# Optimization experiments

Measured on AMD Instinct MI355X. Metric: run time of the kernel, lower is better.

## Reference

```python
import jax, jax.numpy as jnp
import numpy as np
import math

NUM_HEADS = 8

def setup_inputs() -> dict:
    key = jax.random.key(0)
    k1, k2, k3 = jax.random.split(key, 3)
    B, N, C = 16, 4096, 512
    x = jax.random.normal(k1, (B, N, C), dtype=jnp.float32)
    qkv_w = jax.random.normal(k2, (3 * C, C), dtype=jnp.float32) * 0.02
    proj_w = jax.random.normal(k3, (C, C), dtype=jnp.float32) * 0.02
    proj_b = jnp.zeros((C,), dtype=jnp.float32)
    return {"x": x, "qkv_w": qkv_w, "proj_w": proj_w, "proj_b": proj_b}


def reference(x, qkv_w, proj_w, proj_b):
    # Attention with is_mask=1: row-wise windowed attention.
    B, N, C = x.shape
    H = W = int(math.isqrt(N))
    nh = NUM_HEADS
    hd = C // nh
    scale = hd ** (-0.5)

    # fold rows into batch: (B*H, W, C)
    img = x.reshape(B * H, W, C)
    # qkv linear (no bias): (B*H, W, 3C) -> (3, B*H, nh, W, hd)
    qkv = jnp.einsum('bwc,dc->bwd', img, qkv_w)
    qkv = qkv.reshape(B * H, W, 3, nh, hd).transpose(2, 0, 3, 1, 4)
    q, k, v = qkv[0], qkv[1], qkv[2]

    # scaled dot-product attention within each row window
    attn = jnp.einsum('bhqd,bhkd->bhqk', q, k) * scale
    attn = jax.nn.softmax(attn, axis=-1)
    out = jnp.einsum('bhqk,bhkd->bhqd', attn, v)   # (B*H, nh, W, hd)
    out = out.transpose(0, 2, 1, 3).reshape(B, N, C)

    # output projection
    return jnp.einsum('bnc,dc->bnd', out, proj_w) + proj_b
```

## Files before the change

kernel.cpp:

```cpp
#include <hip/hip_runtime.h>
#include <cstdint>
#include <cstddef>

typedef _Float16 half8 __attribute__((ext_vector_type(8)));
typedef _Float16 half4 __attribute__((ext_vector_type(4)));
typedef float f32x4 __attribute__((ext_vector_type(4)));

#define GLDS16(g, l) __builtin_amdgcn_global_load_lds( \
    (__attribute__((address_space(1))) void*)(g), \
    (__attribute__((address_space(3))) void*)(l), 16, 0, 0)

__global__ __launch_bounds__(256) void cvt_f32_f16(const float* __restrict__ src,
                                                   _Float16* __restrict__ dst, int n) {
  int i = (blockIdx.x * 256 + threadIdx.x) * 8;
  if (i >= n) return;
  float4 a = *(const float4*)(src + i);
  float4 b = *(const float4*)(src + i + 4);
  half8 h;
  h[0] = (_Float16)a.x; h[1] = (_Float16)a.y; h[2] = (_Float16)a.z; h[3] = (_Float16)a.w;
  h[4] = (_Float16)b.x; h[5] = (_Float16)b.y; h[6] = (_Float16)b.z; h[7] = (_Float16)b.w;
  *(half8*)(dst + i) = h;
}

template<int NOUT, int NT, bool BIAS>
__global__ __launch_bounds__(512, 2) void gemm_bt(const _Float16* __restrict__ A,
                                                  const _Float16* __restrict__ Bw,
                                                  const float* __restrict__ bias,
                                                  void* __restrict__ Cout) {
  constexpr int K = 512;
  constexpr int NIT = K / 32;
  __shared__ union {
    _Float16 S[3][2][8192];
    float E[2][16][264];
  } u;
  const int id  = blockIdx.x;
  const int xcd = id & 7;
  const int jj  = id >> 3;
  const int by  = (jj / NT) * 8 + xcd;
  const int bx  = jj % NT;
  const int m_base = by * 256, n_base = bx * 256;

  const int t    = threadIdx.x;
  const int lane = t & 63;
  const int wid  = t >> 6;
  const int wm   = wid & 1;
  const int wn   = wid >> 1;
  const int cl   = lane & 15, q = lane >> 4;

  f32x4 acc[8][4] = {};

  const int s0 = t, s1 = t + 512;
  const int r0 = ((s0 >> 6) << 4) | (s0 & 15), c0 = (s0 >> 4) & 3;
  const int r1 = ((s1 >> 6) << 4) | (s1 & 15), c1 = (s1 >> 4) & 3;
  const _Float16* a0 = A  + (size_t)(m_base + r0) * K + c0 * 8;
  const _Float16* a1 = A  + (size_t)(m_base + r1) * K + c1 * 8;
  const _Float16* b0 = Bw + (size_t)(n_base + r0) * K + c0 * 8;
  const _Float16* b1 = Bw + (size_t)(n_base + r1) * K + c1 * 8;

  const int lane8 = lane * 8;

  auto stage = [&](int kt, int b) {
    const int ko = kt * 32;
    GLDS16(a0 + ko, (char*)&u.S[b][0][0] + s0 * 16);
    GLDS16(a1 + ko, (char*)&u.S[b][0][0] + s1 * 16);
    GLDS16(b0 + ko, (char*)&u.S[b][1][0] + s0 * 16);
    GLDS16(b1 + ko, (char*)&u.S[b][1][0] + s1 * 16);
  };

  stage(0, 0);
  stage(1, 1);

#pragma unroll
  for (int k = 0; k < NIT; ++k) {
    if (k < NIT - 1) asm volatile("s_waitcnt vmcnt(4)" ::: "memory");
    else             asm volatile("s_waitcnt vmcnt(0)" ::: "memory");
    __builtin_amdgcn_s_barrier();
    asm volatile("" ::: "memory");
    if (k < NIT - 2) stage(k + 2, (k + 2) % 3);

    const _Float16* As = &u.S[k % 3][0][0];
    const _Float16* Bs = &u.S[k % 3][1][0];
    half8 af[8], bf[4];
#pragma unroll
    for (int i = 0; i < 8; i++) af[i] = *(const half8*)(As + (wm * 8 + i) * 512 + lane8);
#pragma unroll
    for (int i = 0; i < 4; i++) bf[i] = *(const half8*)(Bs + (wn * 4 + i) * 512 + lane8);
#pragma unroll
    for (int mt = 0; mt < 8; mt++)
#pragma unroll
      for (int nt = 0; nt < 4; nt++)
        acc[mt][nt] = __builtin_amdgcn_mfma_f32_16x16x32_f16(af[mt], bf[nt], acc[mt][nt], 0, 0, 0);
  }
  __syncthreads();

  const int eb = t >> 8;
  const int erow = (t >> 4) & 15;
  const int ecs = t & 15;
#pragma unroll
  for (int j = 0; j < 8; ++j) {
#pragma unroll
    for (int nt = 0; nt < 4; nt++)
#pragma unroll
      for (int r = 0; r < 4; r++)
        u.E[wm][q * 4 + r][wn * 64 + nt * 16 + cl] = acc[j][nt][r];
    __syncthreads();
    const size_t rg = (size_t)(m_base + (eb * 8 + j) * 16 + erow);
#pragma unroll
    for (int jo = 0; jo < 4; jo++) {
      const int cc = (ecs + 16 * jo) * 4;
      float4 e = *(const float4*)&u.E[eb][erow][cc];
      if constexpr (BIAS) {
        const float4 bb = *(const float4*)(bias + n_base + cc);
        e.x += bb.x; e.y += bb.y; e.z += bb.z; e.w += bb.w;
        *(float4*)((float*)Cout + rg * NOUT + n_base + cc) = e;
      } else {
        half4 hv;
        hv[0] = (_Float16)e.x; hv[1] = (_Float16)e.y;
        hv[2] = (_Float16)e.z; hv[3] = (_Float16)e.w;
        *(half4*)((_Float16*)Cout + rg * NOUT + n_base + cc) = hv;
      }
    }
    __syncthreads();
  }
}

__global__ __launch_bounds__(256, 3) void attn_win(const _Float16* __restrict__ QKV,
                                                   _Float16* __restrict__ Out) {
  __shared__ _Float16 Qs[4096];
  __shared__ _Float16 Ks[4096];
  __shared__ _Float16 Vt[64][72];
  __shared__ _Float16 Ps[64][72];
  __shared__ _Float16 Os[64][72];
  const int h = blockIdx.x, b = blockIdx.y;
  const int t = threadIdx.x;
  const int lane = t & 63, wid = t >> 6;
  const int cl = lane & 15, q = lane >> 4;

  {
    const int s0 = t, s1 = t + 256;
    const int r0 = ((s0 >> 7) << 4) | (s0 & 15), ch0 = (s0 >> 4) & 7;
    const int r1 = ((s1 >> 7) << 4) | (s1 & 15), ch1 = (s1 >> 4) & 7;
    const _Float16* g0 = QKV + (size_t)(b * 64 + r0) * 1536 + h * 64 + ch0 * 8;
    const _Float16* g1 = QKV + (size_t)(b * 64 + r1) * 1536 + h * 64 + ch1 * 8;
    GLDS16(g0,       (char*)Qs + s0 * 16);
    GLDS16(g1,       (char*)Qs + s1 * 16);
    GLDS16(g0 + 512, (char*)Ks + s0 * 16);
    GLDS16(g1 + 512, (char*)Ks + s1 * 16);

    const int vj = t & 63, vp = t >> 6;
    const _Float16* vsrc = QKV + (size_t)(b * 64 + vj) * 1536 + 1024 + h * 64 + vp * 16;
    half8 v0 = *(const half8*)vsrc;
    half8 v1 = *(const half8*)(vsrc + 8);
#pragma unroll
    for (int i = 0; i < 8; i++) Vt[vp * 16 + i][vj] = v0[i];
#pragma unroll
    for (int i = 0; i < 8; i++) Vt[vp * 16 + 8 + i][vj] = v1[i];
  }
  __syncthreads();

  const int m0 = wid * 16;
  const int lane8 = lane * 8;

  f32x4 s[4] = {};
#pragma unroll
  for (int ks = 0; ks < 2; ks++) {
    half8 a = *(const half8*)(Qs + wid * 1024 + ks * 512 + lane8);
#pragma unroll
    for (int nt = 0; nt < 4; nt++) {
      half8 bb = *(const half8*)(Ks + nt * 1024 + ks * 512 + lane8);
      s[nt] = __builtin_amdgcn_mfma_f32_16x16x32_f16(a, bb, s[nt], 0, 0, 0);
    }
  }

  constexpr float SC = 0.125f * 1.44269504088896340736f;
#pragma unroll
  for (int r = 0; r < 4; r++) {
    float mx = fmaxf(fmaxf(s[0][r], s[1][r]), fmaxf(s[2][r], s[3][r]));
    mx = fmaxf(mx, __shfl_xor(mx, 1));
    mx = fmaxf(mx, __shfl_xor(mx, 2));
    mx = fmaxf(mx, __shfl_xor(mx, 4));
    mx = fmaxf(mx, __shfl_xor(mx, 8));
    float e[4], ssum = 0.f;
#pragma unroll
    for (int nt = 0; nt < 4; nt++) { e[nt] = exp2f((s[nt][r] - mx) * SC); ssum += e[nt]; }
    ssum += __shfl_xor(ssum, 1);
    ssum += __shfl_xor(ssum, 2);
    ssum += __shfl_xor(ssum, 4);
    ssum += __shfl_xor(ssum, 8);
    float inv = 1.f / ssum;
    const int row = m0 + q * 4 + r;
#pragma unroll
    for (int nt = 0; nt < 4; nt++) Ps[row][nt * 16 + cl] = (_Float16)(e[nt] * inv);
  }
  __syncthreads();

  f32x4 o[4] = {};
#pragma unroll
  for (int ks = 0; ks < 2; ks++) {
    half8 a = *(const half8*)&Ps[m0 + cl][ks * 32 + q * 8];
#pragma unroll
    for (int nt = 0; nt < 4; nt++) {
      half8 bb = *(const half8*)&Vt[nt * 16 + cl][ks * 32 + q * 8];
      o[nt] = __builtin_amdgcn_mfma_f32_16x16x32_f16(a, bb, o[nt], 0, 0, 0);
    }
  }
#pragma unroll
  for (int nt = 0; nt < 4; nt++)
#pragma unroll
    for (int r = 0; r < 4; r++)
      Os[m0 + q * 4 + r][nt * 16 + cl] = (_Float16)o[nt][r];
  __syncthreads();

  {
    const int row = t >> 2, cs = t & 3;
    half8 h0 = *(const half8*)&Os[row][cs * 16];
    half8 h1 = *(const half8*)&Os[row][cs * 16 + 8];
    _Float16* dst = Out + (size_t)(b * 64 + row) * 512 + h * 64 + cs * 16;
    *(half8*)dst = h0;
    *((half8*)dst + 1) = h1;
  }
}

extern "C" void kernel_launch(void* const* d_in, const int* in_sizes, int n_in,
                              void* d_out, int out_size, void* d_ws, size_t ws_size,
                              hipStream_t stream) {
  const float* x      = (const float*)d_in[0];
  const float* qkv_w  = (const float*)d_in[1];
  const float* proj_w = (const float*)d_in[2];
  const float* proj_b = (const float*)d_in[3];
  float* out = (float*)d_out;

  char* ws = (char*)d_ws;
  _Float16* QKVh = (_Float16*)ws;
  _Float16* Xh   = (_Float16*)(ws + 201326592);
  _Float16* Outh = Xh;
  _Float16* Wq   = (_Float16*)(ws + 268435456);
  _Float16* Wp   = (_Float16*)(ws + 270008320);

  cvt_f32_f16<<<16384, 256, 0, stream>>>(x, Xh, 16 * 4096 * 512);
  cvt_f32_f16<<<384, 256, 0, stream>>>(qkv_w, Wq, 1536 * 512);
  cvt_f32_f16<<<128, 256, 0, stream>>>(proj_w, Wp, 512 * 512);
  gemm_bt<1536, 6, false><<<1536, 512, 0, stream>>>(Xh, Wq, nullptr, QKVh);
  attn_win<<<dim3(8, 1024), 256, 0, stream>>>(QKVh, Outh);
  gemm_bt<512, 2, true><<<512, 512, 0, stream>>>(Outh, Wp, proj_b, out);
}
```

Before: 480.0 us.

## Restructure GEMM main loop into 8-phase ping-pong schedule with K=64 tiles

Rewrites the GEMM main loop to use a double-buffered K=64 tile instead of a triple-buffered K=32 tile. Each K step is split into four quadrant MFMA phases, with A/B staging loads interleaved between them. Barriers and s_setprio bracket the MFMA bursts, in the style of HipKittens 8-wave ping-pong. Epilogue __syncthreads are replaced by lgkmcnt waits plus raw barriers. The aim is better overlap of global→LDS loads and LDS reads with MFMA work, and fewer barriers per FLOP. In exchange it adds more barriers per iteration and tricky vmcnt accounting, which risks races or stalls.

```diff
diff --git a/kernel.cpp b/kernel.cpp
--- a/kernel.cpp
+++ b/kernel.cpp
@@ -9,6 +9,17 @@
 #define GLDS16(g, l) __builtin_amdgcn_global_load_lds( \
     (__attribute__((address_space(1))) void*)(g), \
     (__attribute__((address_space(3))) void*)(l), 16, 0, 0)
+
+#define LBAR() do { asm volatile("s_waitcnt lgkmcnt(0)" ::: "memory"); \
+                    __builtin_amdgcn_s_barrier(); } while (0)
+
+#define PH_MID() do { __builtin_amdgcn_sched_barrier(0); \
+                      __builtin_amdgcn_s_barrier(); \
+                      __builtin_amdgcn_sched_barrier(0); \
+                      __builtin_amdgcn_s_setprio(1); } while (0)
+#define PH_END() do { __builtin_amdgcn_s_setprio(0); \
+                      __builtin_amdgcn_sched_barrier(0); \
+                      __builtin_amdgcn_s_barrier(); } while (0)
 
 __global__ __launch_bounds__(256) void cvt_f32_f16(const float* __restrict__ src,
                                                    _Float16* __restrict__ dst, int n) {
@@ -28,9 +39,8 @@
                                                   const float* __restrict__ bias,
                                                   void* __restrict__ Cout) {
   constexpr int K = 512;
-  constexpr int NIT = K / 32;
   __shared__ union {
-    _Float16 S[3][2][8192];
+    _Float16 S[2][2][16384];
     float E[2][16][264];
   } u;
   const int id  = blockIdx.x;
@@ -49,49 +59,89 @@
 
   f32x4 acc[8][4] = {};
 
-  const int s0 = t, s1 = t + 512;
-  const int r0 = ((s0 >> 6) << 4) | (s0 & 15), c0 = (s0 >> 4) & 3;
-  const int r1 = ((s1 >> 6) << 4) | (s1 & 15), c1 = (s1 >> 4) & 3;
-  const _Float16* a0 = A  + (size_t)(m_base + r0) * K + c0 * 8;
-  const _Float16* a1 = A  + (size_t)(m_base + r1) * K + c1 * 8;
-  const _Float16* b0 = Bw + (size_t)(n_base + r0) * K + c0 * 8;
-  const _Float16* b1 = Bw + (size_t)(n_base + r1) * K + c1 * 8;
-
-  const int lane8 = lane * 8;
-
-  auto stage = [&](int kt, int b) {
-    const int ko = kt * 32;
-    GLDS16(a0 + ko, (char*)&u.S[b][0][0] + s0 * 16);
-    GLDS16(a1 + ko, (char*)&u.S[b][0][0] + s1 * 16);
-    GLDS16(b0 + ko, (char*)&u.S[b][1][0] + s0 * 16);
-    GLDS16(b1 + ko, (char*)&u.S[b][1][0] + s1 * 16);
+  const int r0 = ((t >> 7) << 4) | (t & 15);
+  const int c0 = (t >> 4) & 7;
+  const _Float16* aR = A  + (size_t)(m_base + r0) * K + c0 * 8;
+  const _Float16* bR = Bw + (size_t)(n_base + r0) * K + c0 * 8;
+  char* Sb = (char*)&u.S[0][0][0];
+
+  auto stageA = [&](int p, int h, int kt) {
+    char* dst = Sb + p * 65536 + h * 16384 + t * 16;
+    const _Float16* s = aR + (size_t)(h * 128) * K + kt * 64;
+    GLDS16(s, dst);
+    GLDS16(s + (size_t)64 * K, dst + 8192);
   };
-
-  stage(0, 0);
-  stage(1, 1);
-
-#pragma unroll
-  for (int k = 0; k < NIT; ++k) {
-    if (k < NIT - 1) asm volatile("s_waitcnt vmcnt(4)" ::: "memory");
-    else             asm volatile("s_waitcnt vmcnt(0)" ::: "memory");
+  auto stageB = [&](int p, int h, int kt) {
+    char* dst = Sb + p * 65536 + 32768 + h * 16384 + t * 16;
+    const _Float16* s = bR + (size_t)(h * 128) * K + kt * 64;
+    GLDS16(s, dst);
+    GLDS16(s + (size_t)64 * K, dst + 8192);
+  };
+
+#define QUAD(AM, BN, BF) \
+  _Pragma("unroll") for (int i_ = 0; i_ < 4; ++i_) \
+  _Pragma("unroll") for (int j_ = 0; j_ < 2; ++j_) \
+  _Pragma("unroll") for (int kk_ = 0; kk_ < 2; ++kk_) \
+    acc[(AM)*4 + i_][(BN)*2 + j_] = __builtin_amdgcn_mfma_f32_16x16x32_f16( \
+        af[i_][kk_], BF[j_][kk_], acc[(AM)*4 + i_][(BN)*2 + j_], 0, 0, 0);
+
+  stageA(0, 0, 0); stageA(0, 1, 0); stageB(0, 0, 0); stageB(0, 1, 0);
+  stageB(1, 0, 1); stageB(1, 1, 1);
+  asm volatile("s_waitcnt vmcnt(4)" ::: "memory");
+  __builtin_amdgcn_s_barrier();
+
+  half8 af[4][2], bf0[2][2], bf1[2][2];
+#pragma unroll
+  for (int c = 0; c < 8; ++c) {
+    const int p = c & 1;
+    const char* aB = (const char*)u.S[p][0] + wm * 16384 + lane * 16;
+    const char* bB = (const char*)u.S[p][1] + wn * 8192 + lane * 16;
+
+#pragma unroll
+    for (int fm = 0; fm < 4; ++fm)
+#pragma unroll
+      for (int kk = 0; kk < 2; ++kk)
+        af[fm][kk] = *(const half8*)(aB + fm * 2048 + kk * 1024);
+#pragma unroll
+    for (int fn = 0; fn < 2; ++fn)
+#pragma unroll
+      for (int kk = 0; kk < 2; ++kk)
+        bf0[fn][kk] = *(const half8*)(bB + fn * 2048 + kk * 1024);
+    if (c + 1 < 8) stageA(p ^ 1, 0, c + 1);
+    PH_MID();
+    QUAD(0, 0, bf0);
+    PH_END();
+
+#pragma unroll
+    for (int fn = 0; fn < 2; ++fn)
+#pragma unroll
+      for (int kk = 0; kk < 2; ++kk)
+        bf1[fn][kk] = *(const half8*)(bB + (2 + fn) * 2048 + kk * 1024);
+    if (c + 1 < 8) stageA(p ^ 1, 1, c + 1);
+    PH_MID();
+    QUAD(0, 1, bf1);
+    PH_END();
+
+#pragma unroll
+    for (int fm = 0; fm < 4; ++fm)
+#pragma unroll
+      for (int kk = 0; kk < 2; ++kk)
+        af[fm][kk] = *(const half8*)(aB + (4 + fm) * 2048 + kk * 1024);
+    if (c + 2 < 8) stageB(p, 0, c + 2);
+    PH_MID();
+    QUAD(1, 1, bf1);
+    PH_END();
+
+    if (c + 2 < 8) stageB(p, 1, c + 2);
+    PH_MID();
+    QUAD(1, 0, bf0);
+    __builtin_amdgcn_s_setprio(0);
+    __builtin_amdgcn_sched_barrier(0);
+    if (c < 6)       { asm volatile("s_waitcnt vmcnt(4)" ::: "memory"); }
+    else if (c == 6) { asm volatile("s_waitcnt vmcnt(0)" ::: "memory"); }
     __builtin_amdgcn_s_barrier();
-    asm volatile("" ::: "memory");
-    if (k < NIT - 2) stage(k + 2, (k + 2) % 3);
-
-    const _Float16* As = &u.S[k % 3][0][0];
-    const _Float16* Bs = &u.S[k % 3][1][0];
-    half8 af[8], bf[4];
-#pragma unroll
-    for (int i = 0; i < 8; i++) af[i] = *(const half8*)(As + (wm * 8 + i) * 512 + lane8);
-#pragma unroll
-    for (int i = 0; i < 4; i++) bf[i] = *(const half8*)(Bs + (wn * 4 + i) * 512 + lane8);
-#pragma unroll
-    for (int mt = 0; mt < 8; mt++)
-#pragma unroll
-      for (int nt = 0; nt < 4; nt++)
-        acc[mt][nt] = __builtin_amdgcn_mfma_f32_16x16x32_f16(af[mt], bf[nt], acc[mt][nt], 0, 0, 0);
-  }
-  __syncthreads();
+  }
+#undef QUAD
 
   const int eb = t >> 8;
   const int erow = (t >> 4) & 15;
@@ -103,7 +153,7 @@
 #pragma unroll
       for (int r = 0; r < 4; r++)
         u.E[wm][q * 4 + r][wn * 64 + nt * 16 + cl] = acc[j][nt][r];
-    __syncthreads();
+    LBAR();
     const size_t rg = (size_t)(m_base + (eb * 8 + j) * 16 + erow);
 #pragma unroll
     for (int jo = 0; jo < 4; jo++) {
@@ -120,7 +170,7 @@
         *(half4*)((_Float16*)Cout + rg * NOUT + n_base + cc) = hv;
       }
     }
-    __syncthreads();
+    LBAR();
   }
 }
 
```

After: 481.1 us. No clear change (+0.2%).
